# Kernel optimization log

Measured on AMD Instinct MI355X. Metric: run time of the kernel, lower is better.

The kernel has to match this reference:

```python
import jax, jax.numpy as jnp
import numpy as np

N_NODES = 100000
N_EDGES = 600000


def gcn_conv(x, W, b, src, dst, ew):
    """PyG GCNConv with edge weights: sym-normalized A-hat (self loops weight 1), then +bias."""
    n = x.shape[0]
    # degree includes self-loop weight 1.0
    deg = jnp.zeros((n,), x.dtype).at[dst].add(ew) + 1.0
    dinv = jax.lax.rsqrt(deg)                      # deg > 0 always (self loop)
    norm = dinv[src] * ew * dinv[dst]              # [E]
    h = x @ W                                      # [n, out]
    agg = jax.ops.segment_sum(h[src] * norm[:, None], dst, num_segments=n)
    agg = agg + h * (dinv * dinv)[:, None]         # self-loop contribution (weight 1)
    return agg + b


def setup_inputs() -> dict:
    key = jax.random.key(0)
    ks = jax.random.split(key, 16)
    x = jax.random.normal(ks[0], (N_NODES, 8), dtype=jnp.float32)
    edge_index = jax.random.randint(ks[1], (2, N_EDGES), 0, N_NODES, dtype=jnp.int32)
    edge_weight = jax.random.uniform(ks[2], (N_EDGES,), dtype=jnp.float32)
    batch = jnp.zeros((N_NODES,), dtype=jnp.int32)  # single graph
    C2ER = jax.random.normal(ks[3], (4,), dtype=jnp.float32)

    def lin(k, fan_in, fan_out):
        kw, kb = jax.random.split(k)
        s = 1.0 / np.sqrt(fan_in)
        W = jax.random.uniform(kw, (fan_in, fan_out), jnp.float32, -s, s)
        b = jax.random.uniform(kb, (fan_out,), jnp.float32, -s, s)
        return W, b

    W1, b1 = lin(ks[4], 8, 32)
    W2, b2 = lin(ks[5], 32, 128)
    W3, b3 = lin(ks[6], 128, 128)
    W4, b4 = lin(ks[7], 128, 32)
    L1W, L1b = lin(ks[8], 68, 128)
    L2W, L2b = lin(ks[9], 128, 128)
    L3W, L3b = lin(ks[10], 128, 10)
    return dict(x=x, edge_index=edge_index, edge_weight=edge_weight, batch=batch, C2ER=C2ER,
                W1=W1, b1=b1, W2=W2, b2=b2, W3=W3, b3=b3, W4=W4, b4=b4,
                L1W=L1W, L1b=L1b, L2W=L2W, L2b=L2b, L3W=L3W, L3b=L3b)


def reference(x, edge_index, edge_weight, batch, C2ER,
              W1, b1, W2, b2, W3, b3, W4, b4,
              L1W, L1b, L2W, L2b, L3W, L3b):
    src, dst = edge_index[0], edge_index[1]
    # dropout is inference-mode identity
    h = jax.nn.relu(gcn_conv(x, W1, b1, src, dst, edge_weight))
    x0 = jax.ops.segment_max(h, batch, num_segments=1)          # [1, 32]
    h = jax.nn.relu(gcn_conv(h, W2, b2, src, dst, edge_weight))
    h = jax.nn.relu(gcn_conv(h, W3, b3, src, dst, edge_weight))
    h = jax.nn.relu(gcn_conv(h, W4, b4, src, dst, edge_weight))
    x1 = jax.ops.segment_max(h, batch, num_segments=1)          # [1, 32]
    code = jnp.concatenate([x0, x1, C2ER.reshape(1, 4)], axis=1)  # [1, 68]
    z = jax.nn.relu(code @ L1W + L1b)
    z = jax.nn.relu(z @ L2W + L2b)
    out = jax.nn.softmax(z @ L3W + L3b, axis=1)                  # [1, 10]
    return out, code
```

## Files before the change

### kernel.cpp

```cpp
#include <hip/hip_runtime.h>
#include <hip/hip_bf16.h>

#define NN 100000
#define NE 600000
#define PAD 40

using bf16 = __hip_bfloat16;
typedef float f32x4 __attribute__((ext_vector_type(4)));
typedef short s16x8 __attribute__((ext_vector_type(8)));

__device__ __forceinline__ float bu2f(unsigned int u16) {
    union { float f; unsigned int i; } c; c.i = u16 << 16; return c.f;
}
__device__ __forceinline__ unsigned int f2bu(float f) {
    bf16 h = __float2bfloat16(f);
    return (unsigned int)*reinterpret_cast<unsigned short*>(&h);
}
__device__ __forceinline__ uint2 st4bf(float4 a) {
    uint2 u;
    u.x = f2bu(a.x) | (f2bu(a.y) << 16);
    u.y = f2bu(a.z) | (f2bu(a.w) << 16);
    return u;
}
__device__ __forceinline__ void up8(uint4 u, float* a) {
    a[0] = bu2f(u.x & 0xffffu); a[1] = bu2f(u.x >> 16);
    a[2] = bu2f(u.y & 0xffffu); a[3] = bu2f(u.y >> 16);
    a[4] = bu2f(u.z & 0xffffu); a[5] = bu2f(u.z >> 16);
    a[6] = bu2f(u.w & 0xffffu); a[7] = bu2f(u.w >> 16);
}

__global__ void k_prep(int* cnt, float* x0x1,
                       const float* W2, const float* W3, const float* W4,
                       short* Wt2, short* Wt3, short* Wt4) {
    int i = blockIdx.x * 256 + threadIdx.x;
    if (i < NN) cnt[i] = 0;
    if (i < 64) x0x1[i] = 0.0f;
    if (i < 4096) {
        int n = i >> 5, k = i & 31;
        Wt2[n * 32 + k] = (short)f2bu(W2[k * 128 + n]);
    }
    if (i >= 4096 && i < 20480) {
        int j = i - 4096; int n = j >> 7, k = j & 127;
        Wt3[n * 128 + k] = (short)f2bu(W3[k * 128 + n]);
    }
    if (i >= 20480 && i < 24576) {
        int j = i - 20480; int n = j >> 7, k = j & 127;
        Wt4[n * 128 + k] = (short)f2bu(W4[k * 32 + n]);
    }
}

__global__ void k_fill(const int* srcI, const int* dstI, const float* ew,
                       int* cnt, uint2* edges) {
    int e = blockIdx.x * 256 + threadIdx.x;
    if (e >= NE) return;
    int d = dstI[e];
    int r = atomicAdd(&cnt[d], 1);
    if (r < PAD)
        edges[(size_t)d * PAD + r] = make_uint2((unsigned)srcI[e], __float_as_uint(ew[e]));
}

__global__ void k_deg(int* cnt, const uint2* edges, float* dinv) {
    int n = blockIdx.x * 256 + threadIdx.x;
    if (n >= NN) return;
    int len = cnt[n];
    if (len > PAD) { len = PAD; cnt[n] = PAD; }
    const uint2* row = edges + (size_t)n * PAD;
    float s = 1.0f;
    for (int i = 0; i < len; i++) s += __uint_as_float(row[i].y);
    dinv[n] = rsqrtf(s);
}

__global__ void k_norm(const int* cnt, const float* dinv, uint2* edges) {
    int n = blockIdx.x * 256 + threadIdx.x;
    if (n >= NN) return;
    float dn = dinv[n];
    int len = cnt[n];
    float* wf = (float*)(edges + (size_t)n * PAD);
    const uint2* row = edges + (size_t)n * PAD;
    for (int i = 0; i < len; i++) {
        uint2 e = row[i];
        wf[2 * i + 1] = __uint_as_float(e.y) * dinv[e.x] * dn;
    }
}

__global__ __launch_bounds__(256) void k_ag8(const float* __restrict__ hin,
        const float* __restrict__ dinv, const int* __restrict__ cnt,
        const uint2* __restrict__ edges, float* __restrict__ outF) {
    int tid = blockIdx.x * 256 + threadIdx.x;
    int n = tid >> 1, g = tid & 1;
    if (n >= NN) return;
    float di = dinv[n];
    float d2 = di * di;
    const float4* h4 = (const float4*)hin;
    float4 s4 = h4[(size_t)n * 2 + g];
    float4 acc = make_float4(s4.x * d2, s4.y * d2, s4.z * d2, s4.w * d2);
    int len = cnt[n];
    const uint2* row = edges + (size_t)n * PAD;
    int i = 0;
    for (; i + 2 <= len; i += 2) {
        uint2 e0 = row[i], e1 = row[i + 1];
        float w0 = __uint_as_float(e0.y), w1 = __uint_as_float(e1.y);
        float4 v0 = h4[(size_t)e0.x * 2 + g];
        float4 v1 = h4[(size_t)e1.x * 2 + g];
        acc.x = fmaf(w0, v0.x, acc.x); acc.y = fmaf(w0, v0.y, acc.y);
        acc.z = fmaf(w0, v0.z, acc.z); acc.w = fmaf(w0, v0.w, acc.w);
        acc.x = fmaf(w1, v1.x, acc.x); acc.y = fmaf(w1, v1.y, acc.y);
        acc.z = fmaf(w1, v1.z, acc.z); acc.w = fmaf(w1, v1.w, acc.w);
    }
    if (i < len) {
        uint2 e0 = row[i];
        float w0 = __uint_as_float(e0.y);
        float4 v0 = h4[(size_t)e0.x * 2 + g];
        acc.x = fmaf(w0, v0.x, acc.x); acc.y = fmaf(w0, v0.y, acc.y);
        acc.z = fmaf(w0, v0.z, acc.z); acc.w = fmaf(w0, v0.w, acc.w);
    }
    ((float4*)outF)[(size_t)n * 2 + g] = acc;
}

__global__ __launch_bounds__(256) void k_gemm8(const float* __restrict__ hin,
                                               const float* __restrict__ Wf,
                                               unsigned int* __restrict__ hW,
                                               const float* __restrict__ bias,
                                               float* xmax) {
    __shared__ float xs[256 * 12];
    __shared__ int smax[32];
    const int base = blockIdx.x * 256;
    const int t = threadIdx.x;
#pragma unroll
    for (int i = 0; i < 2; i++) {
        int idx = t + 256 * i;
        int row = idx >> 1, k4 = idx & 1;
        int node = base + row;
        if (node >= NN) node = NN - 1;
        float4 v = ((const float4*)hin)[(size_t)node * 2 + k4];
        *(float4*)&xs[row * 12 + 4 * k4] = v;
    }
    if (t < 32) smax[t] = 0;
    __syncthreads();
    const int cg = t & 7, ng = t >> 3;
    float4 acc[8];
#pragma unroll
    for (int i = 0; i < 8; i++) acc[i] = make_float4(0.f, 0.f, 0.f, 0.f);
    const float4* wr = (const float4*)Wf;
#pragma unroll
    for (int k = 0; k < 8; k++) {
        float4 w = wr[k * 8 + cg];
#pragma unroll
        for (int i = 0; i < 8; i++) {
            float xv = xs[(ng * 8 + i) * 12 + k];
            acc[i].x = fmaf(xv, w.x, acc[i].x);
            acc[i].y = fmaf(xv, w.y, acc[i].y);
            acc[i].z = fmaf(xv, w.z, acc[i].z);
            acc[i].w = fmaf(xv, w.w, acc[i].w);
        }
    }
    float4 bb = ((const float4*)bias)[cg];
    float4 mx = make_float4(0.f, 0.f, 0.f, 0.f);
#pragma unroll
    for (int i = 0; i < 8; i++) {
        int node = base + ng * 8 + i;
        acc[i].x = fmaxf(acc[i].x + bb.x, 0.f);
        acc[i].y = fmaxf(acc[i].y + bb.y, 0.f);
        acc[i].z = fmaxf(acc[i].z + bb.z, 0.f);
        acc[i].w = fmaxf(acc[i].w + bb.w, 0.f);
        mx.x = fmaxf(mx.x, acc[i].x); mx.y = fmaxf(mx.y, acc[i].y);
        mx.z = fmaxf(mx.z, acc[i].z); mx.w = fmaxf(mx.w, acc[i].w);
        if (node < NN) ((uint2*)hW)[(size_t)node * 8 + cg] = st4bf(acc[i]);
    }
    atomicMax(&smax[cg * 4 + 0], __float_as_int(mx.x));
    atomicMax(&smax[cg * 4 + 1], __float_as_int(mx.y));
    atomicMax(&smax[cg * 4 + 2], __float_as_int(mx.z));
    atomicMax(&smax[cg * 4 + 3], __float_as_int(mx.w));
    __syncthreads();
    if (t < 32) atomicMax((int*)&xmax[t], smax[t]);
}

template<int K, int NOUT, int EPI>
__global__ __launch_bounds__(256) void k_mgemm(const short* __restrict__ A,
                                               const short* __restrict__ Wt,
                                               unsigned short* __restrict__ Out,
                                               const float* __restrict__ bias) {
    constexpr int KS = K / 32;
    constexpr int NT = NOUT / 16;
    const int wave = threadIdx.x >> 6;
    const int lane = threadIdx.x & 63;
    const int m = lane & 15, quad = lane >> 4;
    const int base = blockIdx.x * 64 + wave * 16;
    int anode = base + m;
    if (anode >= NN) anode = NN - 1;
    s16x8 a[KS];
#pragma unroll
    for (int s = 0; s < KS; s++)
        a[s] = *(const s16x8*)(A + ((size_t)anode * K + s * 32 + quad * 8));
    f32x4 acc[NT];
#pragma unroll
    for (int t = 0; t < NT; t++) {
        acc[t] = (f32x4){0.f, 0.f, 0.f, 0.f};
#pragma unroll
        for (int s = 0; s < KS; s++) {
            s16x8 b = *(const s16x8*)(Wt + ((size_t)(t * 16 + m) * K + s * 32 + quad * 8));
            acc[t] = __builtin_amdgcn_mfma_f32_16x16x32_bf16(a[s], b, acc[t], 0, 0, 0);
        }
    }
    const int orow = base + quad * 4;
#pragma unroll
    for (int t = 0; t < NT; t++) {
        float bb = (EPI == 1) ? bias[t * 16 + m] : 0.f;
#pragma unroll
        for (int r = 0; r < 4; r++) {
            int nd = orow + r;
            if (nd < NN) {
                float v = acc[t][r];
                if (EPI == 1) v = fmaxf(v + bb, 0.f);
                Out[(size_t)nd * NOUT + t * 16 + m] = (unsigned short)f2bu(v);
            }
        }
    }
}

template<int W, int EPI>
__global__ __launch_bounds__(256) void k_ag16(const uint4* __restrict__ hin,
        const float* __restrict__ dinv, const int* __restrict__ cnt,
        const uint2* __restrict__ edges, const float* __restrict__ bias,
        uint4* __restrict__ outB, float* __restrict__ xmax) {
    constexpr int TPN = W / 8;
    __shared__ int smax[(EPI == 3) ? W : 1];
    int tid = blockIdx.x * 256 + threadIdx.x;
    int n = tid / TPN, c = tid % TPN;
    if (EPI == 3) {
        if (threadIdx.x < W) smax[threadIdx.x] = 0;
        __syncthreads();
    }
    float acc[8];
    bool valid = (n < NN);
    if (valid) {
        float di = dinv[n];
        float d2 = di * di;
        float a[8];
        up8(hin[(size_t)n * TPN + c], a);
#pragma unroll
        for (int j = 0; j < 8; j++) acc[j] = a[j] * d2;
        int len = cnt[n];
        const uint2* row = edges + (size_t)n * PAD;
        int i = 0;
        for (; i + 2 <= len; i += 2) {
            uint2 e0 = row[i], e1 = row[i + 1];
            float w0 = __uint_as_float(e0.y), w1 = __uint_as_float(e1.y);
            uint4 u0 = hin[(size_t)e0.x * TPN + c];
            uint4 u1 = hin[(size_t)e1.x * TPN + c];
            float a0[8], a1[8];
            up8(u0, a0); up8(u1, a1);
#pragma unroll
            for (int j = 0; j < 8; j++) acc[j] = fmaf(w0, a0[j], acc[j]);
#pragma unroll
            for (int j = 0; j < 8; j++) acc[j] = fmaf(w1, a1[j], acc[j]);
        }
        if (i < len) {
            uint2 e0 = row[i];
            float w0 = __uint_as_float(e0.y);
            float a0[8];
            up8(hin[(size_t)e0.x * TPN + c], a0);
#pragma unroll
            for (int j = 0; j < 8; j++) acc[j] = fmaf(w0, a0[j], acc[j]);
        }
        if (EPI >= 1) {
#pragma unroll
            for (int j = 0; j < 8; j++) acc[j] = fmaxf(acc[j] + bias[c * 8 + j], 0.f);
        }
        if (EPI != 3) {
            uint4 o;
            o.x = f2bu(acc[0]) | (f2bu(acc[1]) << 16);
            o.y = f2bu(acc[2]) | (f2bu(acc[3]) << 16);
            o.z = f2bu(acc[4]) | (f2bu(acc[5]) << 16);
            o.w = f2bu(acc[6]) | (f2bu(acc[7]) << 16);
            outB[(size_t)n * TPN + c] = o;
        } else {
#pragma unroll
            for (int j = 0; j < 8; j++) atomicMax(&smax[c * 8 + j], __float_as_int(acc[j]));
        }
    }
    if (EPI == 3) {
        __syncthreads();
        if (threadIdx.x < W) atomicMax((int*)&xmax[threadIdx.x], smax[threadIdx.x]);
    }
}

__global__ void k_mlp(const float* x0x1, const float* C2,
                      const float* L1W, const float* L1b,
                      const float* L2W, const float* L2b,
                      const float* L3W, const float* L3b, float* out) {
    __shared__ float code[68], z1[128], z2[128];
    int t = threadIdx.x;
    if (t < 64) code[t] = x0x1[t];
    else if (t < 68) code[t] = C2[t - 64];
    __syncthreads();
    float acc = L1b[t];
    for (int i = 0; i < 68; i++) acc = fmaf(code[i], L1W[i * 128 + t], acc);
    z1[t] = fmaxf(acc, 0.f);
    __syncthreads();
    acc = L2b[t];
    for (int i = 0; i < 128; i++) acc = fmaf(z1[i], L2W[i * 128 + t], acc);
    z2[t] = fmaxf(acc, 0.f);
    __syncthreads();
    if (t == 0) {
        float lg[10];
        for (int c = 0; c < 10; c++) {
            float a = L3b[c];
            for (int i = 0; i < 128; i++) a = fmaf(z2[i], L3W[i * 10 + c], a);
            lg[c] = a;
        }
        float m = lg[0];
        for (int c = 1; c < 10; c++) m = fmaxf(m, lg[c]);
        float s = 0.f;
        for (int c = 0; c < 10; c++) { lg[c] = __expf(lg[c] - m); s += lg[c]; }
        float inv = 1.f / s;
        for (int c = 0; c < 10; c++) out[c] = lg[c] * inv;
    }
    if (t < 68) out[10 + t] = code[t];
}

extern "C" void kernel_launch(void* const* d_in, const int* in_sizes, int n_in,
                              void* d_out, int out_size, void* d_ws, size_t ws_size,
                              hipStream_t stream) {
    const float* x   = (const float*)d_in[0];
    const int*   ei  = (const int*)d_in[1];
    const float* ew  = (const float*)d_in[2];
    const float* C2  = (const float*)d_in[4];
    const float* W1  = (const float*)d_in[5],  * b1 = (const float*)d_in[6];
    const float* W2  = (const float*)d_in[7],  * b2 = (const float*)d_in[8];
    const float* W3  = (const float*)d_in[9],  * b3 = (const float*)d_in[10];
    const float* W4  = (const float*)d_in[11], * b4 = (const float*)d_in[12];
    const float* L1W = (const float*)d_in[13], * L1b = (const float*)d_in[14];
    const float* L2W = (const float*)d_in[15], * L2b = (const float*)d_in[16];
    const float* L3W = (const float*)d_in[17], * L3b = (const float*)d_in[18];
    float* out = (float*)d_out;
    (void)in_sizes; (void)n_in; (void)out_size; (void)ws_size;

    const size_t szF = (size_t)NN * 128 * 4;
    char* p = (char*)d_ws;
    char* H       = p;          p += szF;
    char* T       = p;          p += szF;
    uint2* edges  = (uint2*)p;  p += (size_t)NN * PAD * 8;
    float* dinv   = (float*)p;  p += (size_t)NN * 4;
    int*   cnt    = (int*)p;    p += (size_t)NN * 4;
    float* x0x1   = (float*)p;  p += 256 * 4;
    short* Wt2    = (short*)p;  p += 4096 * 2;
    short* Wt3    = (short*)p;  p += 16384 * 2;
    short* Wt4    = (short*)p;  p += 4096 * 2;

    const int* srcI = ei;
    const int* dstI = ei + NE;

    dim3 B(256);
    k_prep<<<dim3((NN + 255) / 256), B, 0, stream>>>(cnt, x0x1, W2, W3, W4, Wt2, Wt3, Wt4);
    k_fill<<<dim3((NE + 255) / 256), B, 0, stream>>>(srcI, dstI, ew, cnt, edges);
    k_deg<<<dim3((NN + 255) / 256), B, 0, stream>>>(cnt, edges, dinv);
    k_norm<<<dim3((NN + 255) / 256), B, 0, stream>>>(cnt, dinv, edges);

    const int MG = (NN + 63) / 64;

    k_ag8<<<dim3((NN * 2 + 255) / 256), B, 0, stream>>>(x, dinv, cnt, edges, (float*)T);
    k_gemm8<<<dim3((NN + 255) / 256), B, 0, stream>>>((const float*)T, W1, (unsigned int*)H, b1, x0x1);
    k_ag16<32, 0><<<dim3((NN * 4 + 255) / 256), B, 0, stream>>>(
        (const uint4*)H, dinv, cnt, edges, nullptr, (uint4*)T, nullptr);
    k_mgemm<32, 128, 1><<<dim3(MG), B, 0, stream>>>((const short*)T, Wt2, (unsigned short*)H, b2);
    k_mgemm<128, 128, 0><<<dim3(MG), B, 0, stream>>>((const short*)H, Wt3, (unsigned short*)T, nullptr);
    k_ag16<128, 1><<<dim3((NN * 16 + 255) / 256), B, 0, stream>>>(
        (const uint4*)T, dinv, cnt, edges, b3, (uint4*)H, nullptr);
    k_mgemm<128, 32, 0><<<dim3(MG), B, 0, stream>>>((const short*)H, Wt4, (unsigned short*)T, nullptr);
    k_ag16<32, 3><<<dim3((NN * 4 + 255) / 256), B, 0, stream>>>(
        (const uint4*)T, dinv, cnt, edges, b4, nullptr, x0x1 + 32);

    k_mlp<<<dim3(1), dim3(128), 0, stream>>>(x0x1, C2, L1W, L1b, L2W, L2b, L3W, L3b, out);
}
```

Before: 313.6 us.

## Factor symmetric normalization into per-node scaling and fuse layer-2 aggregate with GEMM

Rewrites the normalized aggregation D^-1/2 (A+I) D^-1/2 H by pre-scaling node features by dinv and post-scaling aggregated sums by dinv. This drops the k_norm pass that rewrote every edge weight, since raw edge weights are now used directly. Layer-2 aggregation and its 32->128 GEMM are fused into one 1024-thread kernel through shared memory, which avoids writing and re-reading the intermediate. The dinv scaling moves into GEMM and aggregation epilogues, which adds extra per-node loads and an additional bf16 rounding point.

```diff
diff --git a/kernel.cpp b/kernel.cpp
--- a/kernel.cpp
+++ b/kernel.cpp
@@ -59,7 +59,8 @@
         edges[(size_t)d * PAD + r] = make_uint2((unsigned)srcI[e], __float_as_uint(ew[e]));
 }
 
-__global__ void k_deg(int* cnt, const uint2* edges, float* dinv) {
+__global__ void k_deg(int* cnt, const uint2* edges, float* dinv,
+                      const float* x, float* xs) {
     int n = blockIdx.x * 256 + threadIdx.x;
     if (n >= NN) return;
     int len = cnt[n];
@@ -67,33 +68,25 @@
     const uint2* row = edges + (size_t)n * PAD;
     float s = 1.0f;
     for (int i = 0; i < len; i++) s += __uint_as_float(row[i].y);
-    dinv[n] = rsqrtf(s);
-}
-
-__global__ void k_norm(const int* cnt, const float* dinv, uint2* edges) {
-    int n = blockIdx.x * 256 + threadIdx.x;
-    if (n >= NN) return;
-    float dn = dinv[n];
-    int len = cnt[n];
-    float* wf = (float*)(edges + (size_t)n * PAD);
-    const uint2* row = edges + (size_t)n * PAD;
-    for (int i = 0; i < len; i++) {
-        uint2 e = row[i];
-        wf[2 * i + 1] = __uint_as_float(e.y) * dinv[e.x] * dn;
-    }
-}
-
-__global__ __launch_bounds__(256) void k_ag8(const float* __restrict__ hin,
+    float di = rsqrtf(s);
+    dinv[n] = di;
+    const float4* x4 = (const float4*)x;
+    float4 a = x4[(size_t)n * 2], b = x4[(size_t)n * 2 + 1];
+    a.x *= di; a.y *= di; a.z *= di; a.w *= di;
+    b.x *= di; b.y *= di; b.z *= di; b.w *= di;
+    ((float4*)xs)[(size_t)n * 2] = a;
+    ((float4*)xs)[(size_t)n * 2 + 1] = b;
+}
+
+__global__ __launch_bounds__(256) void k_ag8(const float* __restrict__ xs,
         const float* __restrict__ dinv, const int* __restrict__ cnt,
         const uint2* __restrict__ edges, float* __restrict__ outF) {
     int tid = blockIdx.x * 256 + threadIdx.x;
     int n = tid >> 1, g = tid & 1;
     if (n >= NN) return;
-    float di = dinv[n];
-    float d2 = di * di;
-    const float4* h4 = (const float4*)hin;
+    const float4* h4 = (const float4*)xs;
     float4 s4 = h4[(size_t)n * 2 + g];
-    float4 acc = make_float4(s4.x * d2, s4.y * d2, s4.z * d2, s4.w * d2);
+    float4 acc = s4;
     int len = cnt[n];
     const uint2* row = edges + (size_t)n * PAD;
     int i = 0;
@@ -114,11 +107,14 @@
         acc.x = fmaf(w0, v0.x, acc.x); acc.y = fmaf(w0, v0.y, acc.y);
         acc.z = fmaf(w0, v0.z, acc.z); acc.w = fmaf(w0, v0.w, acc.w);
     }
+    float dn = dinv[n];
+    acc.x *= dn; acc.y *= dn; acc.z *= dn; acc.w *= dn;
     ((float4*)outF)[(size_t)n * 2 + g] = acc;
 }
 
 __global__ __launch_bounds__(256) void k_gemm8(const float* __restrict__ hin,
                                                const float* __restrict__ Wf,
+                                               const float* __restrict__ dinv,
                                                unsigned int* __restrict__ hW,
                                                const float* __restrict__ bias,
                                                float* xmax) {
@@ -165,7 +161,11 @@
         acc[i].w = fmaxf(acc[i].w + bb.w, 0.f);
         mx.x = fmaxf(mx.x, acc[i].x); mx.y = fmaxf(mx.y, acc[i].y);
         mx.z = fmaxf(mx.z, acc[i].z); mx.w = fmaxf(mx.w, acc[i].w);
-        if (node < NN) ((uint2*)hW)[(size_t)node * 8 + cg] = st4bf(acc[i]);
+        if (node < NN) {
+            float dn = dinv[node];
+            float4 sc = make_float4(acc[i].x * dn, acc[i].y * dn, acc[i].z * dn, acc[i].w * dn);
+            ((uint2*)hW)[(size_t)node * 8 + cg] = st4bf(sc);
+        }
     }
     atomicMax(&smax[cg * 4 + 0], __float_as_int(mx.x));
     atomicMax(&smax[cg * 4 + 1], __float_as_int(mx.y));
@@ -175,11 +175,90 @@
     if (t < 32) atomicMax((int*)&xmax[t], smax[t]);
 }
 
+__global__ __launch_bounds__(1024) void k_f2(const uint4* __restrict__ hs1,
+        const float* __restrict__ dinv, const int* __restrict__ cnt,
+        const uint2* __restrict__ edges, const short* __restrict__ Wt2,
+        const float* __restrict__ b2, unsigned short* __restrict__ H2) {
+    __shared__ short xs[256 * 40];
+    const int base = blockIdx.x * 256;
+    const int t = threadIdx.x;
+    {
+        int nl = t >> 2, c = t & 3;
+        int n = base + nl;
+        float acc[8] = {0.f, 0.f, 0.f, 0.f, 0.f, 0.f, 0.f, 0.f};
+        if (n < NN) {
+            float a[8];
+            up8(hs1[(size_t)n * 4 + c], a);
+#pragma unroll
+            for (int j = 0; j < 8; j++) acc[j] = a[j];
+            int len = cnt[n];
+            const uint2* row = edges + (size_t)n * PAD;
+            int i = 0;
+            for (; i + 2 <= len; i += 2) {
+                uint2 e0 = row[i], e1 = row[i + 1];
+                float w0 = __uint_as_float(e0.y), w1 = __uint_as_float(e1.y);
+                uint4 u0 = hs1[(size_t)e0.x * 4 + c];
+                uint4 u1 = hs1[(size_t)e1.x * 4 + c];
+                float a0[8], a1[8];
+                up8(u0, a0); up8(u1, a1);
+#pragma unroll
+                for (int j = 0; j < 8; j++) acc[j] = fmaf(w0, a0[j], acc[j]);
+#pragma unroll
+                for (int j = 0; j < 8; j++) acc[j] = fmaf(w1, a1[j], acc[j]);
+            }
+            if (i < len) {
+                uint2 e0 = row[i];
+                float w0 = __uint_as_float(e0.y);
+                float a0[8];
+                up8(hs1[(size_t)e0.x * 4 + c], a0);
+#pragma unroll
+                for (int j = 0; j < 8; j++) acc[j] = fmaf(w0, a0[j], acc[j]);
+            }
+            float dn = dinv[n];
+#pragma unroll
+            for (int j = 0; j < 8; j++) acc[j] *= dn;
+        }
+        unsigned int p[4];
+        p[0] = f2bu(acc[0]) | (f2bu(acc[1]) << 16);
+        p[1] = f2bu(acc[2]) | (f2bu(acc[3]) << 16);
+        p[2] = f2bu(acc[4]) | (f2bu(acc[5]) << 16);
+        p[3] = f2bu(acc[6]) | (f2bu(acc[7]) << 16);
+        *(uint4*)&xs[nl * 40 + c * 8] = make_uint4(p[0], p[1], p[2], p[3]);
+    }
+    __syncthreads();
+    {
+        const int wave = t >> 6;
+        const int lane = t & 63;
+        const int m = lane & 15, quad = lane >> 4;
+        s16x8 a = *(const s16x8*)&xs[(wave * 16 + m) * 40 + quad * 8];
+        f32x4 acc[8];
+#pragma unroll
+        for (int nt = 0; nt < 8; nt++) {
+            acc[nt] = (f32x4){0.f, 0.f, 0.f, 0.f};
+            s16x8 b = *(const s16x8*)(Wt2 + (size_t)(nt * 16 + m) * 32 + quad * 8);
+            acc[nt] = __builtin_amdgcn_mfma_f32_16x16x32_bf16(a, b, acc[nt], 0, 0, 0);
+        }
+        const int orow = base + wave * 16 + quad * 4;
+#pragma unroll
+        for (int nt = 0; nt < 8; nt++) {
+            float bb = b2[nt * 16 + m];
+#pragma unroll
+            for (int r = 0; r < 4; r++) {
+                int nd = orow + r;
+                if (nd < NN) {
+                    float v = fmaxf(acc[nt][r] + bb, 0.f);
+                    H2[(size_t)nd * 128 + nt * 16 + m] = (unsigned short)f2bu(v);
+                }
+            }
+        }
+    }
+}
+
 template<int K, int NOUT, int EPI>
 __global__ __launch_bounds__(256) void k_mgemm(const short* __restrict__ A,
                                                const short* __restrict__ Wt,
-                                               unsigned short* __restrict__ Out,
-                                               const float* __restrict__ bias) {
+                                               const float* __restrict__ dinv,
+                                               unsigned short* __restrict__ Out) {
     constexpr int KS = K / 32;
     constexpr int NT = NOUT / 16;
     const int wave = threadIdx.x >> 6;
@@ -203,15 +282,18 @@
         }
     }
     const int orow = base + quad * 4;
+    float dsc[4];
+#pragma unroll
+    for (int r = 0; r < 4; r++)
+        dsc[r] = (EPI == 2 && orow + r < NN) ? dinv[orow + r] : 1.0f;
 #pragma unroll
     for (int t = 0; t < NT; t++) {
-        float bb = (EPI == 1) ? bias[t * 16 + m] : 0.f;
 #pragma unroll
         for (int r = 0; r < 4; r++) {
             int nd = orow + r;
             if (nd < NN) {
                 float v = acc[t][r];
-                if (EPI == 1) v = fmaxf(v + bb, 0.f);
+                if (EPI == 2) v *= dsc[r];
                 Out[(size_t)nd * NOUT + t * 16 + m] = (unsigned short)f2bu(v);
             }
         }
@@ -234,12 +316,10 @@
     float acc[8];
     bool valid = (n < NN);
     if (valid) {
-        float di = dinv[n];
-        float d2 = di * di;
         float a[8];
         up8(hin[(size_t)n * TPN + c], a);
 #pragma unroll
-        for (int j = 0; j < 8; j++) acc[j] = a[j] * d2;
+        for (int j = 0; j < 8; j++) acc[j] = a[j];
         int len = cnt[n];
         const uint2* row = edges + (size_t)n * PAD;
         int i = 0;
@@ -263,11 +343,11 @@
 #pragma unroll
             for (int j = 0; j < 8; j++) acc[j] = fmaf(w0, a0[j], acc[j]);
         }
-        if (EPI >= 1) {
-#pragma unroll
-            for (int j = 0; j < 8; j++) acc[j] = fmaxf(acc[j] + bias[c * 8 + j], 0.f);
-        }
-        if (EPI != 3) {
+        float dn = dinv[n];
+#pragma unroll
+        for (int j = 0; j < 8; j++)
+            acc[j] = fmaxf(fmaf(dn, acc[j], bias[c * 8 + j]), 0.f);
+        if (EPI == 1) {
             uint4 o;
             o.x = f2bu(acc[0]) | (f2bu(acc[1]) << 16);
             o.y = f2bu(acc[2]) | (f2bu(acc[3]) << 16);
@@ -343,6 +423,7 @@
     uint2* edges  = (uint2*)p;  p += (size_t)NN * PAD * 8;
     float* dinv   = (float*)p;  p += (size_t)NN * 4;
     int*   cnt    = (int*)p;    p += (size_t)NN * 4;
+    float* xs     = (float*)p;  p += (size_t)NN * 8 * 4;
     float* x0x1   = (float*)p;  p += 256 * 4;
     short* Wt2    = (short*)p;  p += 4096 * 2;
     short* Wt3    = (short*)p;  p += 16384 * 2;
@@ -354,22 +435,20 @@
     dim3 B(256);
     k_prep<<<dim3((NN + 255) / 256), B, 0, stream>>>(cnt, x0x1, W2, W3, W4, Wt2, Wt3, Wt4);
     k_fill<<<dim3((NE + 255) / 256), B, 0, stream>>>(srcI, dstI, ew, cnt, edges);
-    k_deg<<<dim3((NN + 255) / 256), B, 0, stream>>>(cnt, edges, dinv);
-    k_norm<<<dim3((NN + 255) / 256), B, 0, stream>>>(cnt, dinv, edges);
+    k_deg<<<dim3((NN + 255) / 256), B, 0, stream>>>(cnt, edges, dinv, x, xs);
 
     const int MG = (NN + 63) / 64;
 
-    k_ag8<<<dim3((NN * 2 + 255) / 256), B, 0, stream>>>(x, dinv, cnt, edges, (float*)T);
-    k_gemm8<<<dim3((NN + 255) / 256), B, 0, stream>>>((const float*)T, W1, (unsigned int*)H, b1, x0x1);
-    k_ag16<32, 0><<<dim3((NN * 4 + 255) / 256), B, 0, stream>>>(
-        (const uint4*)H, dinv, cnt, edges, nullptr, (uint4*)T, nullptr);
-    k_mgemm<32, 128, 1><<<dim3(MG), B, 0, stream>>>((const short*)T, Wt2, (unsigned short*)H, b2);
-    k_mgemm<128, 128, 0><<<dim3(MG), B, 0, stream>>>((const short*)H, Wt3, (unsigned short*)T, nullptr);
+    k_ag8<<<dim3((NN * 2 + 255) / 256), B, 0, stream>>>(xs, dinv, cnt, edges, (float*)T);
+    k_gemm8<<<dim3((NN + 255) / 256), B, 0, stream>>>((const float*)T, W1, dinv, (unsigned int*)H, b1, x0x1);
+    k_f2<<<dim3((NN + 255) / 256), dim3(1024), 0, stream>>>(
+        (const uint4*)H, dinv, cnt, edges, Wt2, b2, (unsigned short*)T);
+    k_mgemm<128, 128, 2><<<dim3(MG), B, 0, stream>>>((const short*)T, Wt3, dinv, (unsigned short*)H);
     k_ag16<128, 1><<<dim3((NN * 16 + 255) / 256), B, 0, stream>>>(
-        (const uint4*)T, dinv, cnt, edges, b3, (uint4*)H, nullptr);
-    k_mgemm<128, 32, 0><<<dim3(MG), B, 0, stream>>>((const short*)H, Wt4, (unsigned short*)T, nullptr);
+        (const uint4*)H, dinv, cnt, edges, b3, (uint4*)T, nullptr);
+    k_mgemm<128, 32, 2><<<dim3(MG), B, 0, stream>>>((const short*)T, Wt4, dinv, (unsigned short*)H);
     k_ag16<32, 3><<<dim3((NN * 4 + 255) / 256), B, 0, stream>>>(
-        (const uint4*)T, dinv, cnt, edges, b4, nullptr, x0x1 + 32);
+        (const uint4*)H, dinv, cnt, edges, b4, nullptr, x0x1 + 32);
 
     k_mlp<<<dim3(1), dim3(128), 0, stream>>>(x0x1, C2, L1W, L1b, L2W, L2b, L3W, L3b, out);
 }
```

Result: no change. 309.8 us (-1.2%).
